# Kernel optimization log

Hardware: AMD Instinct MI355X
Metric: run time of the kernel (lower is better)

Reference implementation:

```python
import jax, jax.numpy as jnp
from jax import lax
import numpy as np

BATCH, SEQ_LEN, INPUT_DIM, HIDDEN, NUM_CLASSES = 2048, 512, 1, 1024, 10


def setup_inputs() -> dict:
    key = jax.random.key(0)
    k1, k2, k3, k4 = jax.random.split(key, 4)
    x = jax.random.normal(k1, (BATCH, SEQ_LEN), dtype=jnp.float32)
    # Parameters match torch.randn init; biases start at zero.
    W_hx = jax.random.normal(k2, (INPUT_DIM, HIDDEN), dtype=jnp.float32)
    W_hh = jax.random.normal(k3, (HIDDEN, HIDDEN), dtype=jnp.float32)
    W_ph = jax.random.normal(k4, (HIDDEN, NUM_CLASSES), dtype=jnp.float32)
    b_h = jnp.zeros((HIDDEN,), dtype=jnp.float32)
    b_p = jnp.zeros((NUM_CLASSES,), dtype=jnp.float32)
    return {"x": x, "W_hx": W_hx, "W_hh": W_hh, "W_ph": W_ph, "b_h": b_h, "b_p": b_p}


def reference(x, W_hx, W_hh, W_ph, b_h, b_p):
    # x: [B, T]; each timestep uses a single scalar feature -> [B, 1] @ [1, H]
    B = x.shape[0]
    H = W_hh.shape[0]

    def step(h, x_t):
        # x_t: [B]; h: [B, H]
        h_new = jnp.tanh(x_t[:, None] @ W_hx + h @ W_hh + b_h)
        return h_new, None

    h0 = jnp.zeros((B, H), dtype=x.dtype)
    h_T, _ = lax.scan(step, h0, x.T)  # scan over time (leading axis T)
    # Only the final timestep's projection is returned (matches original loop).
    return h_T @ W_ph + b_p  # [B, num_classes]
```

## Files before the change

### kernel.cpp

```cpp
#include <hip/hip_runtime.h>


#define SEQ   512
#define HID   1024
#define NCLS  10
#define TPB   512
#define ROWS  8
#define CLAMPV 7.99881172180175781f

__device__ __forceinline__ float tanh_win(float x) {
#pragma clang fp contract(off)
    float xc = fminf(fmaxf(x, -CLAMPV), CLAMPV);
    float x2 = xc * xc;
    float p = -2.76076847742355e-16f;
    p = __fmaf_rn(x2, p,  2.00018790482477e-13f);
    p = __fmaf_rn(x2, p, -8.60467152213735e-11f);
    p = __fmaf_rn(x2, p,  5.12229709037114e-08f);
    p = __fmaf_rn(x2, p,  1.48572235717979e-05f);
    p = __fmaf_rn(x2, p,  6.37261928875436e-04f);
    p = __fmaf_rn(x2, p,  4.89352455891786e-03f);
    p = xc * p;
    float q = 1.19825839466702e-06f;
    q = __fmaf_rn(x2, q,  1.18534705686654e-04f);
    q = __fmaf_rn(x2, q,  2.26843463243900e-03f);
    q = __fmaf_rn(x2, q,  4.89352518554385e-03f);
    float r = p / q;
    return (fabsf(x) < 0.0004f) ? x : r;
}

#define MAC4(hv, wv)                              \
    sv.x = __fmaf_rn((hv), (wv).x, sv.x);         \
    sv.y = __fmaf_rn((hv), (wv).y, sv.y);         \
    sv.z = __fmaf_rn((hv), (wv).z, sv.z);         \
    sv.w = __fmaf_rn((hv), (wv).w, sv.w);

#define LOADG(N, P, R0)                                                        \
    N##0 = *reinterpret_cast<const float4*>((P) + ((R0)    ) * HID + c0);      \
    N##1 = *reinterpret_cast<const float4*>((P) + ((R0) + 1) * HID + c0);      \
    N##2 = *reinterpret_cast<const float4*>((P) + ((R0) + 2) * HID + c0);     \
    N##3 = *reinterpret_cast<const float4*>((P) + ((R0) + 3) * HID + c0);

#define FMAG(N, J)                                                             \
    {                                                                          \
        _Pragma("unroll")                                                      \
        for (int r = 0; r < ROWS; ++r) {                                       \
            const float4 ha =                                                  \
                *reinterpret_cast<const float4*>(hj + r * HID + (J));          \
            float4 sv = s[r];                                                  \
            MAC4(ha.x, N##0); MAC4(ha.y, N##1);                                \
            MAC4(ha.z, N##2); MAC4(ha.w, N##3);                                \
            s[r] = sv;                                                         \
        }                                                                      \
    }

#define FINISH_ROW(ROW)                                                        \
    {                                                                          \
        const float4 so = *reinterpret_cast<const float4*>(&sb[(ROW) * HID + c0]); \
        const float xv = xl[(ROW) * SEQ + t];                                  \
        float4 g;                                                              \
        g.x = s[ROW].x + so.x;                                                 \
        g.y = s[ROW].y + so.y;                                                 \
        g.z = s[ROW].z + so.z;                                                 \
        g.w = s[ROW].w + so.w;                                                 \
        float4 hn;                                                             \
        hn.x = tanh_win(__fmaf_rn(xv, w4.x, g.x) + b4.x);                      \
        hn.y = tanh_win(__fmaf_rn(xv, w4.y, g.y) + b4.y);                      \
        hn.z = tanh_win(__fmaf_rn(xv, w4.z, g.z) + b4.z);                      \
        hn.w = tanh_win(__fmaf_rn(xv, w4.w, g.w) + b4.w);                      \
        *reinterpret_cast<float4*>(&hl[(ROW) * HID + c0]) = hn;                \
    }

__launch_bounds__(TPB, 1)
__global__ void rnn_win(const float* __restrict__ x, const float* __restrict__ W_hx,
                        const float* __restrict__ Whh, const float* __restrict__ W_ph,
                        const float* __restrict__ bh, const float* __restrict__ bp,
                        float* __restrict__ out) {
#pragma clang fp contract(off)
    __shared__ float hl[ROWS * HID];
    __shared__ float xl[ROWS * SEQ];
    __shared__ float sb[ROWS * HID];
    const int tid  = threadIdx.x;
    const int blk  = blockIdx.x;
    const int col  = tid & 255;
    const int pp   = tid >> 8;
    const int c0   = col * 4;
    const int row0 = blk * ROWS;

    for (int i = tid; i < ROWS * SEQ; i += TPB) xl[i] = x[(size_t)row0 * SEQ + i];
    for (int i = tid; i < ROWS * HID; i += TPB) hl[i] = 0.0f;

    const float4 w4 = *reinterpret_cast<const float4*>(W_hx + c0);
    const float4 b4 = *reinterpret_cast<const float4*>(bh + c0);
    const unsigned pbase = (unsigned)__builtin_amdgcn_readfirstlane(pp * (512 * HID));
    const float* __restrict__ wp0 = Whh + pbase;
    __syncthreads();

    float4 A0, A1, A2, A3, B0, B1, B2, B3, C0, C1, C2, C3, D0, D1, D2, D3;
    LOADG(A, wp0, 0);
    LOADG(B, wp0, 4);
    LOADG(C, wp0, 8);

    for (int t = 0; t < SEQ; ++t) {
        float4 s[ROWS];
        #pragma unroll
        for (int r = 0; r < ROWS; ++r) s[r] = float4{0.f, 0.f, 0.f, 0.f};

        const float* wp = wp0;
        const float* hj = &hl[pp * 512];
        #pragma unroll 1
        for (int i = 0; i < 31; ++i) {
            LOADG(D, wp, 12);  FMAG(A, 0);
            LOADG(A, wp, 16);  FMAG(B, 4);
            LOADG(B, wp, 20);  FMAG(C, 8);
            LOADG(C, wp, 24);  FMAG(D, 12);
            wp += 16 * HID;
            hj += 16;
        }
        LOADG(D, wp, 12);
        FMAG(A, 0);
        LOADG(A, wp0, 0);
        FMAG(B, 4);
        LOADG(B, wp0, 4);
        FMAG(C, 8);
        LOADG(C, wp0, 8);
        FMAG(D, 12);

        if (pp == 0) {
            *reinterpret_cast<float4*>(&sb[4 * HID + c0]) = s[4];
            *reinterpret_cast<float4*>(&sb[5 * HID + c0]) = s[5];
            *reinterpret_cast<float4*>(&sb[6 * HID + c0]) = s[6];
            *reinterpret_cast<float4*>(&sb[7 * HID + c0]) = s[7];
        } else {
            *reinterpret_cast<float4*>(&sb[0 * HID + c0]) = s[0];
            *reinterpret_cast<float4*>(&sb[1 * HID + c0]) = s[1];
            *reinterpret_cast<float4*>(&sb[2 * HID + c0]) = s[2];
            *reinterpret_cast<float4*>(&sb[3 * HID + c0]) = s[3];
        }
        __syncthreads();

        if (pp == 0) {
            FINISH_ROW(0); FINISH_ROW(1); FINISH_ROW(2); FINISH_ROW(3);
        } else {
            FINISH_ROW(4); FINISH_ROW(5); FINISH_ROW(6); FINISH_ROW(7);
        }
        __syncthreads();
    }

    if (tid < ROWS * NCLS) {
        const int r = tid / NCLS, k = tid - r * NCLS;
        float acc = bp[k];
        for (int j = 0; j < HID; ++j)
            acc = __fmaf_rn(hl[r * HID + j], W_ph[j * NCLS + k], acc);
        out[(size_t)(row0 + r) * NCLS + k] = acc;
    }
}

extern "C" void kernel_launch(void* const* d_in, const int* in_sizes, int n_in,
                              void* d_out, int out_size, void* d_ws, size_t ws_size,
                              hipStream_t stream) {
    const float* x    = (const float*)d_in[0];
    const float* W_hx = (const float*)d_in[1];
    const float* Whh  = (const float*)d_in[2];
    const float* W_ph = (const float*)d_in[3];
    const float* bh   = (const float*)d_in[4];
    const float* bp   = (const float*)d_in[5];
    float* out = (float*)d_out;

    rnn_win<<<2048 / ROWS, TPB, 0, stream>>>(x, W_hx, Whh, W_ph, bh, bp, out);
}
```

Measured before the change: 32.28 ms.

## Halve block threads and widen per-thread column tile to eight outputs

Each thread now computes 8 hidden columns instead of 4, with 256 threads per block instead of 512. Every shared-memory h load now feeds twice as many FMAs, so LDS traffic per FLOP drops and register-level reuse rises. The W_hh prefetch pipeline is rebuilt as a three-group rotation with a copy at the start of each timestep. The cost is much higher register pressure and fewer waves per CU to hide global-load latency, which could cause spills or stalls.

```diff
diff --git a/kernel.cpp b/kernel.cpp
--- a/kernel.cpp
+++ b/kernel.cpp
@@ -4,7 +4,7 @@
 #define SEQ   512
 #define HID   1024
 #define NCLS  10
-#define TPB   512
+#define TPB   256
 #define ROWS  8
 #define CLAMPV 7.99881172180175781f
 
@@ -28,17 +28,21 @@
     return (fabsf(x) < 0.0004f) ? x : r;
 }
 
-#define MAC4(hv, wv)                              \
-    sv.x = __fmaf_rn((hv), (wv).x, sv.x);         \
-    sv.y = __fmaf_rn((hv), (wv).y, sv.y);         \
-    sv.z = __fmaf_rn((hv), (wv).z, sv.z);         \
+#define MAC4V(hv, wv, sv)                          \
+    sv.x = __fmaf_rn((hv), (wv).x, sv.x);          \
+    sv.y = __fmaf_rn((hv), (wv).y, sv.y);          \
+    sv.z = __fmaf_rn((hv), (wv).z, sv.z);          \
     sv.w = __fmaf_rn((hv), (wv).w, sv.w);
 
 #define LOADG(N, P, R0)                                                        \
-    N##0 = *reinterpret_cast<const float4*>((P) + ((R0)    ) * HID + c0);      \
-    N##1 = *reinterpret_cast<const float4*>((P) + ((R0) + 1) * HID + c0);      \
-    N##2 = *reinterpret_cast<const float4*>((P) + ((R0) + 2) * HID + c0);     \
-    N##3 = *reinterpret_cast<const float4*>((P) + ((R0) + 3) * HID + c0);
+    N##00 = *reinterpret_cast<const float4*>((P) + ((R0)    ) * HID + c0);     \
+    N##01 = *reinterpret_cast<const float4*>((P) + ((R0)    ) * HID + c0 + 4); \
+    N##10 = *reinterpret_cast<const float4*>((P) + ((R0) + 1) * HID + c0);     \
+    N##11 = *reinterpret_cast<const float4*>((P) + ((R0) + 1) * HID + c0 + 4); \
+    N##20 = *reinterpret_cast<const float4*>((P) + ((R0) + 2) * HID + c0);     \
+    N##21 = *reinterpret_cast<const float4*>((P) + ((R0) + 2) * HID + c0 + 4); \
+    N##30 = *reinterpret_cast<const float4*>((P) + ((R0) + 3) * HID + c0);     \
+    N##31 = *reinterpret_cast<const float4*>((P) + ((R0) + 3) * HID + c0 + 4);
 
 #define FMAG(N, J)                                                             \
     {                                                                          \
@@ -46,28 +50,44 @@
         for (int r = 0; r < ROWS; ++r) {                                       \
             const float4 ha =                                                  \
                 *reinterpret_cast<const float4*>(hj + r * HID + (J));          \
-            float4 sv = s[r];                                                  \
-            MAC4(ha.x, N##0); MAC4(ha.y, N##1);                                \
-            MAC4(ha.z, N##2); MAC4(ha.w, N##3);                                \
-            s[r] = sv;                                                         \
+            float4 sa = s0[r], sbv = s1[r];                                    \
+            MAC4V(ha.x, N##00, sa); MAC4V(ha.x, N##01, sbv);                   \
+            MAC4V(ha.y, N##10, sa); MAC4V(ha.y, N##11, sbv);                   \
+            MAC4V(ha.z, N##20, sa); MAC4V(ha.z, N##21, sbv);                   \
+            MAC4V(ha.w, N##30, sa); MAC4V(ha.w, N##31, sbv);                   \
+            s0[r] = sa; s1[r] = sbv;                                           \
         }                                                                      \
     }
 
-#define FINISH_ROW(ROW)                                                        \
+#define ACOPY()                                                                \
+    A00 = C00; A01 = C01; A10 = C10; A11 = C11;                                \
+    A20 = C20; A21 = C21; A30 = C30; A31 = C31;
+
+#define PUBROW(R)                                                              \
+    *reinterpret_cast<float4*>(&sb[(R) * HID + c0])     = s0[R];               \
+    *reinterpret_cast<float4*>(&sb[(R) * HID + c0 + 4]) = s1[R];
+
+#define FINISH_ROW(R)                                                          \
     {                                                                          \
-        const float4 so = *reinterpret_cast<const float4*>(&sb[(ROW) * HID + c0]); \
-        const float xv = xl[(ROW) * SEQ + t];                                  \
-        float4 g;                                                              \
-        g.x = s[ROW].x + so.x;                                                 \
-        g.y = s[ROW].y + so.y;                                                 \
-        g.z = s[ROW].z + so.z;                                                 \
-        g.w = s[ROW].w + so.w;                                                 \
-        float4 hn;                                                             \
-        hn.x = tanh_win(__fmaf_rn(xv, w4.x, g.x) + b4.x);                      \
-        hn.y = tanh_win(__fmaf_rn(xv, w4.y, g.y) + b4.y);                      \
-        hn.z = tanh_win(__fmaf_rn(xv, w4.z, g.z) + b4.z);                      \
-        hn.w = tanh_win(__fmaf_rn(xv, w4.w, g.w) + b4.w);                      \
-        *reinterpret_cast<float4*>(&hl[(ROW) * HID + c0]) = hn;                \
+        const float4 so0 = *reinterpret_cast<const float4*>(&sb[(R) * HID + c0]);     \
+        const float4 so1 = *reinterpret_cast<const float4*>(&sb[(R) * HID + c0 + 4]); \
+        const float xv = xl[(R) * SEQ + t];                                    \
+        float4 g0, g1;                                                         \
+        g0.x = s0[R].x + so0.x; g0.y = s0[R].y + so0.y;                        \
+        g0.z = s0[R].z + so0.z; g0.w = s0[R].w + so0.w;                        \
+        g1.x = s1[R].x + so1.x; g1.y = s1[R].y + so1.y;                        \
+        g1.z = s1[R].z + so1.z; g1.w = s1[R].w + so1.w;                        \
+        float4 h0, h1;                                                         \
+        h0.x = tanh_win(__fmaf_rn(xv, wqa.x, g0.x) + bqa.x);                   \
+        h0.y = tanh_win(__fmaf_rn(xv, wqa.y, g0.y) + bqa.y);                   \
+        h0.z = tanh_win(__fmaf_rn(xv, wqa.z, g0.z) + bqa.z);                   \
+        h0.w = tanh_win(__fmaf_rn(xv, wqa.w, g0.w) + bqa.w);                   \
+        h1.x = tanh_win(__fmaf_rn(xv, wqb.x, g1.x) + bqb.x);                   \
+        h1.y = tanh_win(__fmaf_rn(xv, wqb.y, g1.y) + bqb.y);                   \
+        h1.z = tanh_win(__fmaf_rn(xv, wqb.z, g1.z) + bqb.z);                   \
+        h1.w = tanh_win(__fmaf_rn(xv, wqb.w, g1.w) + bqb.w);                   \
+        *reinterpret_cast<float4*>(&hl[(R) * HID + c0])     = h0;              \
+        *reinterpret_cast<float4*>(&hl[(R) * HID + c0 + 4]) = h1;              \
     }
 
 __launch_bounds__(TPB, 1)
@@ -81,60 +101,56 @@
     __shared__ float sb[ROWS * HID];
     const int tid  = threadIdx.x;
     const int blk  = blockIdx.x;
-    const int col  = tid & 255;
-    const int pp   = tid >> 8;
-    const int c0   = col * 4;
+    const int col  = tid & 127;
+    const int pp   = tid >> 7;
+    const int c0   = col * 8;
     const int row0 = blk * ROWS;
 
     for (int i = tid; i < ROWS * SEQ; i += TPB) xl[i] = x[(size_t)row0 * SEQ + i];
     for (int i = tid; i < ROWS * HID; i += TPB) hl[i] = 0.0f;
 
-    const float4 w4 = *reinterpret_cast<const float4*>(W_hx + c0);
-    const float4 b4 = *reinterpret_cast<const float4*>(bh + c0);
+    const float4 wqa = *reinterpret_cast<const float4*>(W_hx + c0);
+    const float4 wqb = *reinterpret_cast<const float4*>(W_hx + c0 + 4);
+    const float4 bqa = *reinterpret_cast<const float4*>(bh + c0);
+    const float4 bqb = *reinterpret_cast<const float4*>(bh + c0 + 4);
     const unsigned pbase = (unsigned)__builtin_amdgcn_readfirstlane(pp * (512 * HID));
     const float* __restrict__ wp0 = Whh + pbase;
     __syncthreads();
 
-    float4 A0, A1, A2, A3, B0, B1, B2, B3, C0, C1, C2, C3, D0, D1, D2, D3;
-    LOADG(A, wp0, 0);
-    LOADG(B, wp0, 4);
-    LOADG(C, wp0, 8);
+    float4 A00, A01, A10, A11, A20, A21, A30, A31;
+    float4 B00, B01, B10, B11, B20, B21, B30, B31;
+    float4 C00, C01, C10, C11, C20, C21, C30, C31;
+    LOADG(C, wp0, 0);
 
     for (int t = 0; t < SEQ; ++t) {
-        float4 s[ROWS];
+        ACOPY();
+        LOADG(B, wp0, 4);
+
+        float4 s0[ROWS], s1[ROWS];
         #pragma unroll
-        for (int r = 0; r < ROWS; ++r) s[r] = float4{0.f, 0.f, 0.f, 0.f};
+        for (int r = 0; r < ROWS; ++r) {
+            s0[r] = float4{0.f, 0.f, 0.f, 0.f};
+            s1[r] = float4{0.f, 0.f, 0.f, 0.f};
+        }
 
         const float* wp = wp0;
         const float* hj = &hl[pp * 512];
         #pragma unroll 1
-        for (int i = 0; i < 31; ++i) {
-            LOADG(D, wp, 12);  FMAG(A, 0);
-            LOADG(A, wp, 16);  FMAG(B, 4);
-            LOADG(B, wp, 20);  FMAG(C, 8);
-            LOADG(C, wp, 24);  FMAG(D, 12);
-            wp += 16 * HID;
-            hj += 16;
+        for (int i = 0; i < 42; ++i) {
+            LOADG(C, wp, 8);   FMAG(A, 0);
+            LOADG(A, wp, 12);  FMAG(B, 4);
+            LOADG(B, wp, 16);  FMAG(C, 8);
+            wp += 12 * HID;
+            hj += 12;
         }
-        LOADG(D, wp, 12);
+        LOADG(C, wp0, 0);
         FMAG(A, 0);
-        LOADG(A, wp0, 0);
         FMAG(B, 4);
-        LOADG(B, wp0, 4);
-        FMAG(C, 8);
-        LOADG(C, wp0, 8);
-        FMAG(D, 12);
 
         if (pp == 0) {
-            *reinterpret_cast<float4*>(&sb[4 * HID + c0]) = s[4];
-            *reinterpret_cast<float4*>(&sb[5 * HID + c0]) = s[5];
-            *reinterpret_cast<float4*>(&sb[6 * HID + c0]) = s[6];
-            *reinterpret_cast<float4*>(&sb[7 * HID + c0]) = s[7];
+            PUBROW(4); PUBROW(5); PUBROW(6); PUBROW(7);
         } else {
-            *reinterpret_cast<float4*>(&sb[0 * HID + c0]) = s[0];
-            *reinterpret_cast<float4*>(&sb[1 * HID + c0]) = s[1];
-            *reinterpret_cast<float4*>(&sb[2 * HID + c0]) = s[2];
-            *reinterpret_cast<float4*>(&sb[3 * HID + c0]) = s[3];
+            PUBROW(0); PUBROW(1); PUBROW(2); PUBROW(3);
         }
         __syncthreads();
 
```

Measured after the change: 29.80 ms. 7.7% less time.
